# Optimization experiments

Measured on AMD Instinct MI355X. Metric: run time of the kernel, lower is better.

Reference implementation:

```python
import jax, jax.numpy as jnp
import numpy as np

EPS = 1e-6
NUM_HEADS = 16

def _ln(x):
    m = jnp.mean(x, -1, keepdims=True)
    v = jnp.mean((x - m) ** 2, -1, keepdims=True)
    return (x - m) * jax.lax.rsqrt(v + EPS)

def _rms(x, w):
    return x * jax.lax.rsqrt(jnp.mean(x * x, -1, keepdims=True) + EPS) * w

def _to_mha(t):
    B, S, D = t.shape
    return t.reshape(B, S, NUM_HEADS, D // NUM_HEADS).transpose(0, 2, 1, 3)

def _rope(t, freqs):
    # t: [B,H,T,Hd], freqs: [T, Hd//2, 2] (cos, sin)
    B, H, T, Hd = t.shape
    tr = t.reshape(B, H, T, Hd // 2, 2)
    cos, sin = freqs[..., 0], freqs[..., 1]
    r = tr[..., 0] * cos - tr[..., 1] * sin
    i = tr[..., 0] * sin + tr[..., 1] * cos
    return jnp.stack([r, i], -1).reshape(B, H, T, Hd)

def _pre(h, qk_w, qn, kn, v_w, v_b):
    qk = h @ qk_w.T                      # [B,S,2D], no bias (c_qk bias=False)
    q, k = jnp.split(qk, 2, -1)
    q = _rms(_to_mha(q), qn)             # per-head RMSNorm
    k = _rms(_to_mha(k), kn)
    v = _to_mha(h @ v_w.T + v_b)
    return q, k, v

def _post(x, a, pw, pb, w1, b1, w3, b3, w2, b2):
    x = x + a @ pw.T + pb                # residual + c_proj
    h = _ln(x)
    m = (jax.nn.silu(h @ w1.T + b1) * (h @ w3.T + b3)) @ w2.T + b2  # SwiGLU
    return x + m

def _forward(x, c, freqs, px_qk_w, px_qn, px_kn, px_v_w, px_v_b,
             pc_qk_w, pc_qn, pc_kn, pc_v_w, pc_v_b,
             p1_proj_w, p1_proj_b, p1_w1, p1_b1, p1_w3, p1_b3, p1_w2, p1_b2,
             p2_proj_w, p2_proj_b, p2_w1, p2_b1, p2_w3, p2_b3, p2_w2, p2_b2):
    x_ln, c_ln = _ln(x), _ln(c)
    qc, kc, vc = _pre(c_ln, pc_qk_w, pc_qn, pc_kn, pc_v_w, pc_v_b)
    qx, kx, vx = _pre(x_ln, px_qk_w, px_qn, px_kn, px_v_w, px_v_b)
    q = jnp.concatenate([qc, qx], 2)     # [B,H,T,Hd], T = S+L
    k = jnp.concatenate([kc, kx], 2)
    v = jnp.concatenate([vc, vx], 2)
    q = _rope(q, freqs)
    k = _rope(k, freqs)
    Hd = q.shape[-1]
    scores = jnp.einsum('bhqd,bhkd->bhqk', q, k) / jnp.sqrt(jnp.float32(Hd))
    T = scores.shape[-1]
    causal = jnp.tril(jnp.ones((T, T), bool))
    scores = jnp.where(causal, scores, jnp.finfo(scores.dtype).min)
    p = jax.nn.softmax(scores, -1)
    y = jnp.einsum('bhqk,bhkd->bhqd', p, v)
    B, D = x.shape[0], x.shape[-1]
    y = y.transpose(0, 2, 1, 3).reshape(B, -1, D)  # [B,T,D]
    S = c.shape[1]
    y_c, y_x = y[:, :S], y[:, S:]
    x_out = _post(x, y_x, p1_proj_w, p1_proj_b, p1_w1, p1_b1, p1_w3, p1_b3, p1_w2, p1_b2)
    c_out = _post(c, y_c, p2_proj_w, p2_proj_b, p2_w1, p2_b1, p2_w3, p2_b3, p2_w2, p2_b2)
    return x_out, c_out

def setup_inputs() -> dict:
    B, L, S, D, H, FF = 1, 1536, 512, 1024, 16, 4096
    Hd, T = D // H, L + S
    key = jax.random.key(0)
    ks = iter(jax.random.split(key, 40))
    def rn(shape, s=0.02):
        return (jax.random.normal(next(ks), shape, jnp.float32) * s)
    pos = jnp.arange(T, dtype=jnp.float32)
    inv = 1.0 / (10000.0 ** (jnp.arange(0, Hd, 2, dtype=jnp.float32) / Hd))
    ang = pos[:, None] * inv[None, :]
    freqs = jnp.stack([jnp.cos(ang), jnp.sin(ang)], -1)  # [T, Hd//2, 2]
    inp = {
        'x': jax.random.normal(next(ks), (B, L, D), jnp.float32),
        'c': jax.random.normal(next(ks), (B, S, D), jnp.float32),
        'freqs': freqs,
        'px_qk_w': rn((2 * D, D)), 'px_qn': jnp.ones((Hd,)), 'px_kn': jnp.ones((Hd,)),
        'px_v_w': rn((D, D)), 'px_v_b': rn((D,)),
        'pc_qk_w': rn((2 * D, D)), 'pc_qn': jnp.ones((Hd,)), 'pc_kn': jnp.ones((Hd,)),
        'pc_v_w': rn((D, D)), 'pc_v_b': rn((D,)),
    }
    for pfx in ('p1', 'p2'):
        inp[pfx + '_proj_w'] = rn((D, D)); inp[pfx + '_proj_b'] = rn((D,))
        inp[pfx + '_w1'] = rn((FF, D)); inp[pfx + '_b1'] = rn((FF,))
        inp[pfx + '_w3'] = rn((FF, D)); inp[pfx + '_b3'] = rn((FF,))
        inp[pfx + '_w2'] = rn((D, FF)); inp[pfx + '_b2'] = rn((D,))
    return inp

def reference(x, c, freqs, px_qk_w, px_qn, px_kn, px_v_w, px_v_b,
              pc_qk_w, pc_qn, pc_kn, pc_v_w, pc_v_b,
              p1_proj_w, p1_proj_b, p1_w1, p1_b1, p1_w3, p1_b3, p1_w2, p1_b2,
              p2_proj_w, p2_proj_b, p2_w1, p2_b1, p2_w3, p2_b3, p2_w2, p2_b2):
    return _forward(x, c, freqs, px_qk_w, px_qn, px_kn, px_v_w, px_v_b,
                    pc_qk_w, pc_qn, pc_kn, pc_v_w, pc_v_b,
                    p1_proj_w, p1_proj_b, p1_w1, p1_b1, p1_w3, p1_b3, p1_w2, p1_b2,
                    p2_proj_w, p2_proj_b, p2_w1, p2_b1, p2_w3, p2_b3, p2_w2, p2_b2)
```

## Files before the change

### kernel.cpp

```cpp
#include <hip/hip_runtime.h>

typedef __attribute__((ext_vector_type(8))) short short8;
typedef __attribute__((ext_vector_type(4))) float floatx4;
typedef __attribute__((ext_vector_type(4))) unsigned short ushortx4;

__device__ __forceinline__ float bf2f(unsigned short u) {
  union { unsigned int i; float f; } v; v.i = ((unsigned int)u) << 16; return v.f;
}
__device__ __forceinline__ unsigned short f2bf(float f) {
  union { float f; unsigned int i; } v; v.f = f;
  unsigned int x = v.i + 0x7fffu + ((v.i >> 16) & 1u);
  return (unsigned short)(x >> 16);
}
__device__ __forceinline__ float loadE(const void* p, size_t i, int f) {
  return f ? ((const float*)p)[i] : bf2f(((const unsigned short*)p)[i]);
}
__device__ __forceinline__ uint4 packbf(float4 a, float4 b) {
  union { unsigned short u[8]; uint4 v; } p;
  p.u[0] = f2bf(a.x); p.u[1] = f2bf(a.y); p.u[2] = f2bf(a.z); p.u[3] = f2bf(a.w);
  p.u[4] = f2bf(b.x); p.u[5] = f2bf(b.y); p.u[6] = f2bf(b.z); p.u[7] = f2bf(b.w);
  return p.v;
}

__device__ __forceinline__ void gl16(const unsigned short* g, unsigned short* l) {
  __builtin_amdgcn_global_load_lds(
      (const __attribute__((address_space(1))) void*)g,
      (__attribute__((address_space(3))) void*)l, 16, 0, 0);
}

__global__ void detect_kernel(const unsigned int* __restrict__ probe, int* __restrict__ flag) {
  if (threadIdx.x == 0 && blockIdx.x == 0) *flag = (probe[0] == 0x3F800000u) ? 1 : 0;
}

struct CArgs {
  const void* in[12];
  unsigned short* out[12];
  unsigned int cum[12];
};
__global__ __launch_bounds__(256) void convw_kernel(CArgs a, const int* __restrict__ flagp) {
  const int flag = *flagp;
  int bc = blockIdx.x * 2048;
  int s = 0;
  while (bc >= (int)a.cum[s]) ++s;
  int base = s ? (int)a.cum[s - 1] : 0;
  size_t e0 = ((size_t)(bc - base) + threadIdx.x) * 8;
  if (flag) {
    const float* in = (const float*)a.in[s];
    unsigned short* out = a.out[s];
    float4 v0[8], v1[8];
    #pragma unroll
    for (int k = 0; k < 8; ++k) {
      size_t e = e0 + (size_t)k * 2048;
      v0[k] = *(const float4*)(in + e);
      v1[k] = *(const float4*)(in + e + 4);
    }
    #pragma unroll
    for (int k = 0; k < 8; ++k)
      *(uint4*)(out + e0 + (size_t)k * 2048) = packbf(v0[k], v1[k]);
  } else {
    const unsigned short* in = (const unsigned short*)a.in[s];
    unsigned short* out = a.out[s];
    #pragma unroll
    for (int k = 0; k < 8; ++k) {
      size_t e = e0 + (size_t)k * 2048;
      *(uint4*)(out + e) = *(const uint4*)(in + e);
    }
  }
}

__global__ __launch_bounds__(256) void zero_kernel(void* __restrict__ out, int out_elems,
                                                   const int* __restrict__ flagp) {
  int limit = (*flagp) ? (out_elems >> 2) : (out_elems >> 3);
  int i = blockIdx.x * 256 + threadIdx.x;
  if (i < limit) ((uint4*)out)[i] = make_uint4(0, 0, 0, 0);
}

__global__ __launch_bounds__(256) void reduce_kernel(const float* __restrict__ part,
                                                     const unsigned short* __restrict__ mid,
                                                     const void* __restrict__ b1,
                                                     const void* __restrict__ b2,
                                                     float* __restrict__ out,
                                                     const int* __restrict__ flagp) {
  if (!*flagp) return;
  const size_t TD = 2097152, LD = (size_t)1536 * 1024, SD = (size_t)512 * 1024;
  size_t i = ((size_t)blockIdx.x * 256 + threadIdx.x) * 4;
  if (i >= TD) return;
  float4 v  = *(const float4*)(part + i);
  float4 v1 = *(const float4*)(part + TD + i);
  float4 v2 = *(const float4*)(part + 2 * TD + i);
  float4 v3 = *(const float4*)(part + 3 * TD + i);
  v.x += v1.x + v2.x + v3.x;
  v.y += v1.y + v2.y + v3.y;
  v.z += v1.z + v2.z + v3.z;
  v.w += v1.w + v2.w + v3.w;
  int col = (int)(i & 1023);
  const float* bias = (const float*)((i < LD) ? b1 : b2);
  size_t ri = (i < LD) ? (SD + i) : (i - LD);
  v.x += bias[col + 0] + bf2f(mid[ri + 0]);
  v.y += bias[col + 1] + bf2f(mid[ri + 1]);
  v.z += bias[col + 2] + bf2f(mid[ri + 2]);
  v.w += bias[col + 3] + bf2f(mid[ri + 3]);
  *(float4*)(out + i) = v;
}

__global__ __launch_bounds__(256) void reduce_mid_kernel(const float* __restrict__ part,
                                                         const void* __restrict__ cres,
                                                         const void* __restrict__ xres,
                                                         const float* __restrict__ b_c,
                                                         const float* __restrict__ b_x,
                                                         unsigned short* __restrict__ mid,
                                                         const int* __restrict__ flagp) {
  if (!*flagp) return;
  const size_t TD = 2097152;
  size_t i = ((size_t)blockIdx.x * 256 + threadIdx.x) * 4;
  if (i >= TD) return;
  float4 v  = *(const float4*)(part + i);
  float4 v1 = *(const float4*)(part + TD + i);
  float4 v2 = *(const float4*)(part + 2 * TD + i);
  float4 v3 = *(const float4*)(part + 3 * TD + i);
  v.x += v1.x + v2.x + v3.x;
  v.y += v1.y + v2.y + v3.y;
  v.z += v1.z + v2.z + v3.z;
  v.w += v1.w + v2.w + v3.w;
  int row = (int)(i >> 10), col = (int)(i & 1023);
  const float* bias = (row < 512) ? b_c : b_x;
  const float* res = (row < 512)
      ? (const float*)cres + ((size_t)row << 10) + col
      : (const float*)xres + ((size_t)(row - 512) << 10) + col;
  float4 rv = *(const float4*)res;
  float4 bv = *(const float4*)(bias + col);
  ushortx4 o;
  o[0] = f2bf(v.x + bv.x + rv.x);
  o[1] = f2bf(v.y + bv.y + rv.y);
  o[2] = f2bf(v.z + bv.z + rv.z);
  o[3] = f2bf(v.w + bv.w + rv.w);
  *(ushortx4*)(mid + i) = o;
}

__global__ __launch_bounds__(256) void ln_ext_kernel(const void* __restrict__ cin,
                                                     const void* __restrict__ xin,
                                                     unsigned short* __restrict__ out,
                                                     const int* __restrict__ flagp) {
  const int D = 1024, S = 512;
  const int flag = *flagp;
  int row = blockIdx.x;
  const void* src = (row < S) ? cin : xin;
  size_t rb = (size_t)(row < S ? row : row - S) * D;
  int base = threadIdx.x * 4;
  float x0 = loadE(src, rb + base + 0, flag);
  float x1 = loadE(src, rb + base + 1, flag);
  float x2 = loadE(src, rb + base + 2, flag);
  float x3 = loadE(src, rb + base + 3, flag);
  float s1 = x0 + x1 + x2 + x3;
  float s2 = x0 * x0 + x1 * x1 + x2 * x2 + x3 * x3;
  for (int off = 32; off; off >>= 1) {
    s1 += __shfl_down(s1, off, 64);
    s2 += __shfl_down(s2, off, 64);
  }
  __shared__ float red[8];
  int wid = threadIdx.x >> 6;
  if ((threadIdx.x & 63) == 0) { red[wid] = s1; red[4 + wid] = s2; }
  __syncthreads();
  s1 = red[0] + red[1] + red[2] + red[3];
  s2 = red[4] + red[5] + red[6] + red[7];
  float mean = s1 * (1.0f / D);
  float var = s2 * (1.0f / D) - mean * mean;
  float inv = rsqrtf(var + 1e-6f);
  unsigned short* dst = out + (size_t)row * D + base;
  dst[0] = f2bf((x0 - mean) * inv);
  dst[1] = f2bf((x1 - mean) * inv);
  dst[2] = f2bf((x2 - mean) * inv);
  dst[3] = f2bf((x3 - mean) * inv);
}

__global__ __launch_bounds__(256) void ln_mid_kernel(const unsigned short* __restrict__ in,
                                                     unsigned short* __restrict__ outc,
                                                     unsigned short* __restrict__ outx) {
  const int D = 1024, S = 512;
  int row = blockIdx.x;
  const unsigned short* src = in + (size_t)row * D;
  int base = threadIdx.x * 4;
  float x0 = bf2f(src[base + 0]);
  float x1 = bf2f(src[base + 1]);
  float x2 = bf2f(src[base + 2]);
  float x3 = bf2f(src[base + 3]);
  float s1 = x0 + x1 + x2 + x3;
  float s2 = x0 * x0 + x1 * x1 + x2 * x2 + x3 * x3;
  for (int off = 32; off; off >>= 1) {
    s1 += __shfl_down(s1, off, 64);
    s2 += __shfl_down(s2, off, 64);
  }
  __shared__ float red[8];
  int wid = threadIdx.x >> 6;
  if ((threadIdx.x & 63) == 0) { red[wid] = s1; red[4 + wid] = s2; }
  __syncthreads();
  s1 = red[0] + red[1] + red[2] + red[3];
  s2 = red[4] + red[5] + red[6] + red[7];
  float mean = s1 * (1.0f / D);
  float var = s2 * (1.0f / D) - mean * mean;
  float inv = rsqrtf(var + 1e-6f);
  unsigned short* dst = (row < S ? outc + (size_t)row * D : outx + (size_t)(row - S) * D) + base;
  dst[0] = f2bf((x0 - mean) * inv);
  dst[1] = f2bf((x1 - mean) * inv);
  dst[2] = f2bf((x2 - mean) * inv);
  dst[3] = f2bf((x3 - mean) * inv);
}

struct GArgs {
  const unsigned short* A[4];
  const void* B[4];
  const void* bias[4];
  const void* res[4];
  void* C[4];
  unsigned long long oo[4];
  int mcum[4];
  int N[4];
  int K;
  int nd;
  int tmask;
  float* part;
};

#define BAR() asm volatile("s_waitcnt lgkmcnt(0)\n\ts_barrier" ::: "memory")
#define FBAR() asm volatile("s_waitcnt vmcnt(0) lgkmcnt(0)\n\ts_barrier" ::: "memory")
#define CBAR4() asm volatile("s_waitcnt vmcnt(4) lgkmcnt(0)\n\ts_barrier" ::: "memory")

template <int RES_MODE, int OUT_MODE, int SPLITK, int BBF16>
__global__ __launch_bounds__(256) void gemm_kernel(GArgs g, const int* __restrict__ flagp) {
  const int flag = *flagp;
  int by = blockIdx.y;
  int d = 0;
  while (d < g.nd - 1 && by >= g.mcum[d]) ++d;
  int mbase = (d == 0) ? 0 : g.mcum[d - 1];
  const int m0 = (by - mbase) * 128;
  const int N = g.N[d];
  const int n0 = blockIdx.x * 128;
  if (n0 >= N) return;
  const int K = g.K;
  int kbeg = 0, kend = K;
  if (SPLITK > 1) {
    if (!flag) {
      if (blockIdx.z != 0) return;
    } else {
      int kl = K / SPLITK;
      kbeg = blockIdx.z * kl;
      kend = kbeg + kl;
    }
  }
  const int nt = (kend - kbeg) >> 5;

  constexpr int NBUF = BBF16 ? 3 : 2;
  constexpr int BSTRIDE = BBF16 ? 4096 : 5120;
  __shared__ __align__(16) unsigned short sA[NBUF * BSTRIDE];
  __shared__ __align__(16) unsigned short sB[NBUF * BSTRIDE];

  const int tid = threadIdx.x;
  const int lane = tid & 63;
  const int wave = tid >> 6;
  const int wm = (wave >> 1) * 64, wn = (wave & 1) * 64;
  const int srow = tid >> 2;
  const int scol = BBF16 ? ((((tid & 3) ^ ((tid >> 3) & 3))) * 8) : ((tid & 3) * 8);
  const unsigned short* Ag0 = g.A[d] + (size_t)(m0 + srow) * K + kbeg + scol;
  const unsigned short* Ag1 = Ag0 + (size_t)64 * K;
  const unsigned short* Bh0 = (const unsigned short*)g.B[d] + (size_t)(n0 + srow) * K + kbeg + scol;
  const unsigned short* Bh1 = Bh0 + (size_t)64 * K;

  const int fr = lane & 15;
  const int rdo = BBF16 ? ((((lane >> 4) ^ ((fr >> 1) & 3))) * 8) : ((lane >> 4) * 8);
  constexpr int PITCH = BBF16 ? 32 : 40;
  floatx4 acc[4][4] = {};
  auto compute = [&](const unsigned short* as, const unsigned short* bs) {
    short8 af[4], bfr[4];
    #pragma unroll
    for (int i = 0; i < 4; ++i) {
      af[i]  = *(const short8*)(as + (wm + i * 16 + fr) * PITCH + rdo);
      bfr[i] = *(const short8*)(bs + (wn + i * 16 + fr) * PITCH + rdo);
    }
    #pragma unroll
    for (int mi = 0; mi < 4; ++mi)
      #pragma unroll
      for (int ni = 0; ni < 4; ++ni)
        acc[mi][ni] = __builtin_amdgcn_mfma_f32_16x16x32_bf16(af[mi], bfr[ni], acc[mi][ni], 0, 0, 0);
  };

  if (BBF16) {
    unsigned short* lA0 = sA + wave * 512;
    unsigned short* lA1 = lA0 + 2048;
    unsigned short* lB0 = sB + wave * 512;
    unsigned short* lB1 = lB0 + 2048;
    auto stage = [&](int buf, int kk) {
      int bo = buf * 4096;
      gl16(Ag0 + kk, lA0 + bo);
      gl16(Ag1 + kk, lA1 + bo);
      gl16(Bh0 + kk, lB0 + bo);
      gl16(Bh1 + kk, lB1 + bo);
    };
    stage(0, 0);
    if (nt > 1) stage(1, 32);
    int b = 0;
    for (int t = 0; t < nt; ++t) {
      if (t + 1 < nt) CBAR4();
      else            FBAR();
      int b2 = (b >= 1) ? b - 1 : 2;
      if (t + 2 < nt) stage(b2, (t + 2) * 32);
      compute(sA + b * 4096, sB + b * 4096);
      b = (b == 2) ? 0 : b + 1;
    }
  } else {
    const float* Bf0 = (const float*)g.B[d] + (size_t)(n0 + srow) * K + kbeg + scol;
    const float* Bf1 = Bf0 + (size_t)64 * K;
    const int wo0 = srow * 40 + scol;
    const int wo1 = wo0 + 64 * 40;
    uint4 ra0, ra1, rb0, rb1;
    auto load_tile = [&](int kk) {
      ra0 = *(const uint4*)(Ag0 + kk);
      ra1 = *(const uint4*)(Ag1 + kk);
      if (!flag) {
        rb0 = *(const uint4*)(Bh0 + kk);
        rb1 = *(const uint4*)(Bh1 + kk);
      } else {
        float4 x0 = *(const float4*)(Bf0 + kk), x1 = *(const float4*)(Bf0 + kk + 4);
        float4 y0 = *(const float4*)(Bf1 + kk), y1 = *(const float4*)(Bf1 + kk + 4);
        rb0 = packbf(x0, x1);
        rb1 = packbf(y0, y1);
      }
    };
    auto store_tile = [&](int buf) {
      unsigned short* sa = sA + buf * 5120;
      unsigned short* sb = sB + buf * 5120;
      *(uint4*)(sa + wo0) = ra0;
      *(uint4*)(sa + wo1) = ra1;
      *(uint4*)(sb + wo0) = rb0;
      *(uint4*)(sb + wo1) = rb1;
    };
    load_tile(0);
    store_tile(0);
    if (nt > 1) load_tile(32);
    BAR();
    for (int t = 0; t < nt; ++t) {
      if (t + 1 < nt) {
        store_tile((t + 1) & 1);
        if (t + 2 < nt) load_tile((t + 2) * 32);
      }
      compute(sA + (t & 1) * 5120, sB + (t & 1) * 5120);
      if (t + 1 < nt) BAR();
    }
  }

  const void* bias = g.bias[d];
  const void* res = g.res[d];
  void* C = g.C[d];
  const size_t oo = g.oo[d];
  const bool first = (SPLITK <= 1) || (blockIdx.z == 0) || !flag;
  const bool rawpart = (OUT_MODE == 3) && (flag != 0);
  const bool trans = (OUT_MODE == 0) && (((g.tmask) >> d) & 1);
  #pragma unroll
  for (int mi = 0; mi < 4; ++mi)
    #pragma unroll
    for (int ni = 0; ni < 4; ++ni) {
      int colb = n0 + wn + ni * 16 + (lane & 15);
      int rowb = m0 + wm + mi * 16 + (lane >> 4) * 4;
      if (trans) {
        ushortx4 o4;
        #pragma unroll
        for (int r = 0; r < 4; ++r) {
          float val = acc[mi][ni][r];
          if (bias) val += loadE(bias, (size_t)colb, flag);
          o4[r] = f2bf(val);
        }
        *(ushortx4*)((unsigned short*)C + (size_t)colb * 2048 + oo + rowb) = o4;
      } else {
        #pragma unroll
        for (int r = 0; r < 4; ++r) {
          int row = rowb + r;
          int col = colb;
          float val = acc[mi][ni][r];
          size_t off = (size_t)row * N + col;
          if (first && !rawpart) {
            if (bias) val += loadE(bias, (size_t)col, flag);
            if (RES_MODE == 1) val += loadE(res, off, flag);
            if (RES_MODE == 3) {
              float h1v = bf2f(((const unsigned short*)res)[off]);
              val = (h1v / (1.0f + __expf(-h1v))) * val;
            }
            if (RES_MODE == 4) val += bf2f(((const unsigned short*)res)[off]);
          }
          if (OUT_MODE == 0) {
            ((unsigned short*)C)[off] = f2bf(val);
          } else if (OUT_MODE == 3) {
            if (flag) g.part[(size_t)blockIdx.z * 2097152 + oo + off] = val;
            else      ((unsigned short*)C)[oo + off] = f2bf(val);
          } else {
            if (flag) {
              if (SPLITK > 1) atomicAdd((float*)C + oo + off, val);
              else            ((float*)C)[oo + off] = val;
            } else {
              ((unsigned short*)C)[oo + off] = f2bf(val);
            }
          }
        }
      }
    }
}

__global__ __launch_bounds__(256) void rmsrope_kernel(
    unsigned short* __restrict__ qk,
    const void* __restrict__ qn_c, const void* __restrict__ kn_c,
    const void* __restrict__ qn_x, const void* __restrict__ kn_x,
    const void* __restrict__ freqs, const int* __restrict__ flagp) {
  const int flag = *flagp;
  int t = blockIdx.x;
  int h = blockIdx.y * 4 + (threadIdx.x >> 6);
  int d = threadIdx.x & 63;
  unsigned short* qrow = qk + (size_t)t * 2048 + h * 64;
  unsigned short* krow = qrow + 1024;
  float q = bf2f(qrow[d]), k = bf2f(krow[d]);
  float qs = q * q, ks = k * k;
  for (int off = 32; off; off >>= 1) {
    qs += __shfl_xor(qs, off, 64);
    ks += __shfl_xor(ks, off, 64);
  }
  const void* qn = (t < 512) ? qn_c : qn_x;
  const void* kn = (t < 512) ? kn_c : kn_x;
  q = q * rsqrtf(qs * (1.0f / 64.0f) + 1e-6f) * loadE(qn, d, flag);
  k = k * rsqrtf(ks * (1.0f / 64.0f) + 1e-6f) * loadE(kn, d, flag);
  int j = d >> 1;
  float cv = loadE(freqs, (size_t)(t * 32 + j) * 2 + 0, flag);
  float sv = loadE(freqs, (size_t)(t * 32 + j) * 2 + 1, flag);
  float qo = __shfl_xor(q, 1, 64);
  float ko = __shfl_xor(k, 1, 64);
  float qn2, kn2;
  if ((d & 1) == 0) { qn2 = q * cv - qo * sv; kn2 = k * cv - ko * sv; }
  else              { qn2 = qo * sv + q * cv; kn2 = ko * sv + k * cv; }
  qrow[d] = f2bf(qn2);
  krow[d] = f2bf(kn2);
}

__global__ __launch_bounds__(256) void attn_kernel(const unsigned short* __restrict__ qk,
                                                   const unsigned short* __restrict__ vT,
                                                   unsigned short* __restrict__ y) {
  int id = blockIdx.x;
  int blk = (id & 256) ? (31 - (id & 31)) : (id & 31);
  int h = (id >> 5) & 15;
  int wv = threadIdx.x >> 6;
  int lane = threadIdx.x & 63;
  int qbase = blk * 64 + wv * 16;

  __shared__ __align__(16) unsigned short Ks[2 * 4096];
  __shared__ __align__(16) unsigned short Vs[2 * 4096];
  __shared__ __align__(16) unsigned short ps[4][16 * 72];

  const int c0 = wv * 64 + lane;
  const int r0 = c0 >> 3,         k0 = (c0 & 7) ^ (r0 & 7);
  const int r1 = (c0 + 256) >> 3, k1 = (c0 & 7) ^ (r1 & 7);
  unsigned short* kd0 = Ks + wv * 512;
  unsigned short* kd1 = Ks + 2048 + wv * 512;
  unsigned short* vd0 = Vs + wv * 512;
  unsigned short* vd1 = Vs + 2048 + wv * 512;
  const unsigned short* kgp0 = qk + 1024 + h * 64 + k0 * 8 + (size_t)r0 * 2048;
  const unsigned short* kgp1 = qk + 1024 + h * 64 + k1 * 8 + (size_t)r1 * 2048;
  const unsigned short* vgp0 = vT + (size_t)(h * 64 + r0) * 2048 + k0 * 8;
  const unsigned short* vgp1 = vT + (size_t)(h * 64 + r1) * 2048 + k1 * 8;
  auto stage = [&](int buf, int j0) {
    int bo = buf * 4096;
    gl16(kgp0 + (size_t)j0 * 2048, kd0 + bo);
    gl16(kgp1 + (size_t)j0 * 2048, kd1 + bo);
    gl16(vgp0 + j0, vd0 + bo);
    gl16(vgp1 + j0, vd1 + bo);
  };

  short8 qa[2];
  {
    int m = lane & 15, dj = (lane >> 4) * 8;
    const unsigned short* qp = qk + (size_t)(qbase + m) * 2048 + h * 64 + dj;
    qa[0] = *(const short8*)(qp);
    qa[1] = *(const short8*)(qp + 32);
  }
  floatx4 o[4] = {};
  float mrow[4] = {-1e30f, -1e30f, -1e30f, -1e30f};
  float lrow[4] = {0.f, 0.f, 0.f, 0.f};
  int ntiles = blk + 1;

  stage(0, 0);
  FBAR();
  for (int tile = 0; tile < ntiles; ++tile) {
    int j0 = tile * 64;
    if (tile + 1 < ntiles) stage((tile + 1) & 1, j0 + 64);
    const unsigned short* Kb = Ks + (tile & 1) * 4096;
    const unsigned short* Vb = Vs + (tile & 1) * 4096;
    floatx4 sacc[4];
    #pragma unroll
    for (int kg = 0; kg < 4; ++kg) {
      floatx4 z = {0.f, 0.f, 0.f, 0.f};
      #pragma unroll
      for (int kc = 0; kc < 2; ++kc) {
        int kr = kg * 16 + (lane & 15);
        int p = (kc * 4 + (lane >> 4)) ^ (kr & 7);
        short8 kb = *(const short8*)(Kb + kr * 64 + p * 8);
        z = __builtin_amdgcn_mfma_f32_16x16x32_bf16(qa[kc], kb, z, 0, 0, 0);
      }
      sacc[kg] = z;
    }
    if (tile == blk) {
      #pragma unroll
      for (int kg = 0; kg < 4; ++kg)
        #pragma unroll
        for (int r = 0; r < 4; ++r) {
          int key_g = j0 + kg * 16 + (lane & 15);
          int q_g = qbase + (lane >> 4) * 4 + r;
          float s = sacc[kg][r] * 0.125f;
          sacc[kg][r] = (key_g <= q_g) ? s : -1e30f;
        }
    } else {
      #pragma unroll
      for (int kg = 0; kg < 4; ++kg)
        #pragma unroll
        for (int r = 0; r < 4; ++r) sacc[kg][r] *= 0.125f;
    }
    #pragma unroll
    for (int r = 0; r < 4; ++r) {
      float mx = fmaxf(fmaxf(sacc[0][r], sacc[1][r]), fmaxf(sacc[2][r], sacc[3][r]));
      mx = fmaxf(mx, __shfl_xor(mx, 1, 64));
      mx = fmaxf(mx, __shfl_xor(mx, 2, 64));
      mx = fmaxf(mx, __shfl_xor(mx, 4, 64));
      mx = fmaxf(mx, __shfl_xor(mx, 8, 64));
      float mnew = fmaxf(mrow[r], mx);
      float al = __expf(mrow[r] - mnew);
      mrow[r] = mnew;
      float sum = 0.f;
      #pragma unroll
      for (int kg = 0; kg < 4; ++kg) {
        float p = __expf(sacc[kg][r] - mnew);
        sacc[kg][r] = p;
        sum += p;
      }
      sum += __shfl_xor(sum, 1, 64);
      sum += __shfl_xor(sum, 2, 64);
      sum += __shfl_xor(sum, 4, 64);
      sum += __shfl_xor(sum, 8, 64);
      lrow[r] = lrow[r] * al + sum;
      #pragma unroll
      for (int ni = 0; ni < 4; ++ni) o[ni][r] *= al;
    }
    unsigned short* pw = ps[wv];
    #pragma unroll
    for (int kg = 0; kg < 4; ++kg)
      #pragma unroll
      for (int r = 0; r < 4; ++r)
        pw[((lane >> 4) * 4 + r) * 72 + kg * 16 + (lane & 15)] = f2bf(sacc[kg][r]);
    asm volatile("s_waitcnt lgkmcnt(0)" ::: "memory");
    short8 pa[2];
    pa[0] = *(const short8*)(pw + (lane & 15) * 72 + (lane >> 4) * 8);
    pa[1] = *(const short8*)(pw + (lane & 15) * 72 + 32 + (lane >> 4) * 8);
    #pragma unroll
    for (int ni = 0; ni < 4; ++ni) {
      floatx4 z = o[ni];
      int dd = ni * 16 + (lane & 15);
      #pragma unroll
      for (int kc = 0; kc < 2; ++kc) {
        int p = (kc * 4 + (lane >> 4)) ^ (dd & 7);
        short8 vb = *(const short8*)(Vb + dd * 64 + p * 8);
        z = __builtin_amdgcn_mfma_f32_16x16x32_bf16(pa[kc], vb, z, 0, 0, 0);
      }
      o[ni] = z;
    }
    if (tile + 1 < ntiles) FBAR();
  }
  #pragma unroll
  for (int ni = 0; ni < 4; ++ni)
    #pragma unroll
    for (int r = 0; r < 4; ++r) {
      int q = qbase + (lane >> 4) * 4 + r;
      int dd = ni * 16 + (lane & 15);
      y[(size_t)q * 1024 + h * 64 + dd] = f2bf(o[ni][r] / lrow[r]);
    }
}

extern "C" void kernel_launch(void* const* d_in, const int* in_sizes, int n_in,
                              void* d_out, int out_size, void* d_ws, size_t ws_size,
                              hipStream_t stream) {
  const int L = 1536, S = 512, D = 1024, T = 2048, FF = 4096;
  const void* x        = d_in[0];
  const void* c        = d_in[1];
  const void* freqs    = d_in[2];
  const void* px_qk_w  = d_in[3];
  const void* px_qn    = d_in[4];
  const void* px_kn    = d_in[5];
  const void* px_v_w   = d_in[6];
  const void* px_v_b   = d_in[7];
  const void* pc_qk_w  = d_in[8];
  const void* pc_qn    = d_in[9];
  const void* pc_kn    = d_in[10];
  const void* pc_v_w   = d_in[11];
  const void* pc_v_b   = d_in[12];
  const void* p1_proj_w = d_in[13];
  const void* p1_proj_b = d_in[14];
  const void* p1_w1 = d_in[15];
  const void* p1_b1 = d_in[16];
  const void* p1_w3 = d_in[17];
  const void* p1_b3 = d_in[18];
  const void* p1_w2 = d_in[19];
  const void* p1_b2 = d_in[20];
  const void* p2_proj_w = d_in[21];
  const void* p2_proj_b = d_in[22];
  const void* p2_w1 = d_in[23];
  const void* p2_b1 = d_in[24];
  const void* p2_w3 = d_in[25];
  const void* p2_b3 = d_in[26];
  const void* p2_w2 = d_in[27];
  const void* p2_b2 = d_in[28];

  char* ws = (char*)d_ws;
  unsigned short* hln     = (unsigned short*)(ws);
  unsigned short* ybuf    = (unsigned short*)(ws);
  unsigned short* h1c     = (unsigned short*)(ws);
  unsigned short* qkbuf   = (unsigned short*)(ws + ((size_t)4  << 20));
  unsigned short* h1x     = (unsigned short*)(ws + ((size_t)4  << 20));
  unsigned short* vbufT   = (unsigned short*)(ws + ((size_t)12 << 20));
  unsigned short* mid     = (unsigned short*)(ws + ((size_t)16 << 20));
  unsigned short* midln_c = (unsigned short*)(ws + ((size_t)20 << 20));
  int*            flag    = (int*)(ws + ((size_t)21 << 20));
  unsigned short* midln_x = (unsigned short*)d_out;
  unsigned short* hlnx    = hln + (size_t)S * D;

  const bool conv = ws_size >= ((size_t)90 << 20);
  unsigned short* wbf = (unsigned short*)(ws + ((size_t)24 << 20));
  unsigned short* b_qk_c = wbf + 0;
  unsigned short* b_qk_x = wbf + 2097152;
  unsigned short* b_v_c  = wbf + 4194304;
  unsigned short* b_v_x  = wbf + 5242880;
  unsigned short* b_pj1  = wbf + 6291456;
  unsigned short* b_pj2  = wbf + 7340032;
  unsigned short* b_w1p1 = wbf + 8388608;
  unsigned short* b_w1p2 = wbf + 12582912;
  unsigned short* b_w3p1 = wbf + 16777216;
  unsigned short* b_w3p2 = wbf + 20971520;
  unsigned short* b_w2p1 = wbf + 25165824;
  unsigned short* b_w2p2 = wbf + 29360128;
  float* part = (float*)(ws + ((size_t)40 << 20));

  detect_kernel<<<1, 64, 0, stream>>>((const unsigned int*)px_qn, flag);

  if (conv) {
    CArgs ca = {};
    const void* insA[8]    = {pc_qk_w, px_qk_w, pc_v_w, px_v_w, p1_proj_w, p2_proj_w,
                              p1_w2, p2_w2};
    unsigned short* osA[8] = {b_qk_c, b_qk_x, b_v_c, b_v_x, b_pj1, b_pj2,
                              b_w2p1, b_w2p2};
    unsigned int cntA[8]   = {262144, 262144, 131072, 131072, 131072, 131072,
                              524288, 524288};
    unsigned int cum = 0;
    for (int i = 0; i < 8; ++i) { ca.in[i] = insA[i]; ca.out[i] = osA[i]; cum += cntA[i]; ca.cum[i] = cum; }
    for (int i = 8; i < 12; ++i) ca.cum[i] = 0x7FFFFFFFu;
    convw_kernel<<<1024, 256, 0, stream>>>(ca, flag);
  }

  ln_ext_kernel<<<T, 256, 0, stream>>>(c, x, hln, flag);

  {
    GArgs g = {};
    g.A[0] = hln;  g.bias[0] = nullptr; g.C[0] = qkbuf;                    g.mcum[0] = 4;  g.N[0] = 2048;
    g.A[1] = hlnx; g.bias[1] = nullptr; g.C[1] = qkbuf + (size_t)S * 2048; g.mcum[1] = 16; g.N[1] = 2048;
    g.A[2] = hln;  g.bias[2] = pc_v_b;  g.C[2] = vbufT; g.oo[2] = 0;       g.mcum[2] = 20; g.N[2] = 1024;
    g.A[3] = hlnx; g.bias[3] = px_v_b;  g.C[3] = vbufT; g.oo[3] = S;       g.mcum[3] = 32; g.N[3] = 1024;
    g.K = 1024; g.nd = 4; g.tmask = 0b1100;
    if (conv) {
      g.B[0] = b_qk_c; g.B[1] = b_qk_x; g.B[2] = b_v_c; g.B[3] = b_v_x;
      gemm_kernel<0, 0, 1, 1><<<dim3(16, 32), 256, 0, stream>>>(g, flag);
    } else {
      g.B[0] = pc_qk_w; g.B[1] = px_qk_w; g.B[2] = pc_v_w; g.B[3] = px_v_w;
      gemm_kernel<0, 0, 1, 0><<<dim3(16, 32), 256, 0, stream>>>(g, flag);
    }
  }
  rmsrope_kernel<<<dim3(T, 4), 256, 0, stream>>>(qkbuf, pc_qn, pc_kn, px_qn, px_kn, freqs, flag);
  attn_kernel<<<512, 256, 0, stream>>>(qkbuf, vbufT, ybuf);

  if (conv) {
    GArgs g = {};
    g.A[0] = ybuf;                  g.C[0] = mid; g.oo[0] = 0;             g.bias[0] = p2_proj_b; g.res[0] = c; g.mcum[0] = 4;  g.N[0] = 1024;
    g.A[1] = ybuf + (size_t)S * D;  g.C[1] = mid; g.oo[1] = (size_t)S * D; g.bias[1] = p1_proj_b; g.res[1] = x; g.mcum[1] = 16; g.N[1] = 1024;
    g.K = 1024; g.nd = 2;
    g.part = part;
    g.B[0] = b_pj2; g.B[1] = b_pj1;
    gemm_kernel<1, 3, 4, 1><<<dim3(8, 16, 4), 256, 0, stream>>>(g, flag);
    reduce_mid_kernel<<<2048, 256, 0, stream>>>(part, c, x, (const float*)p2_proj_b,
                                                (const float*)p1_proj_b, mid, flag);
    CArgs cb = {};
    const void* insB[4]    = {p1_w1, p2_w1, p1_w3, p2_w3};
    unsigned short* osB[4] = {b_w1p1, b_w1p2, b_w3p1, b_w3p2};
    unsigned int cum = 0;
    for (int i = 0; i < 4; ++i) { cb.in[i] = insB[i]; cb.out[i] = osB[i]; cum += 524288u; cb.cum[i] = cum; }
    for (int i = 4; i < 12; ++i) cb.cum[i] = 0x7FFFFFFFu;
    convw_kernel<<<1024, 256, 0, stream>>>(cb, flag);
  } else {
    GArgs g = {};
    g.A[0] = ybuf;                  g.bias[0] = p2_proj_b; g.res[0] = c; g.C[0] = mid;                  g.mcum[0] = 4;  g.N[0] = 1024;
    g.A[1] = ybuf + (size_t)S * D;  g.bias[1] = p1_proj_b; g.res[1] = x; g.C[1] = mid + (size_t)S * D;  g.mcum[1] = 16; g.N[1] = 1024;
    g.K = 1024; g.nd = 2;
    g.B[0] = p2_proj_w; g.B[1] = p1_proj_w;
    gemm_kernel<1, 0, 1, 0><<<dim3(8, 16), 256, 0, stream>>>(g, flag);
  }
  ln_mid_kernel<<<T, 256, 0, stream>>>(mid, midln_c, midln_x);

  {
    GArgs g = {};
    g.A[0] = midln_x; g.bias[0] = p1_b1; g.C[0] = h1x; g.mcum[0] = 12; g.N[0] = 4096;
    g.A[1] = midln_c; g.bias[1] = p2_b1; g.C[1] = h1c; g.mcum[1] = 16; g.N[1] = 4096;
    g.K = 1024; g.nd = 2;
    if (conv) {
      g.B[0] = b_w1p1; g.B[1] = b_w1p2;
      gemm_kernel<0, 0, 1, 1><<<dim3(32, 16), 256, 0, stream>>>(g, flag);
    } else {
      g.B[0] = p1_w1; g.B[1] = p2_w1;
      gemm_kernel<0, 0, 1, 0><<<dim3(32, 16), 256, 0, stream>>>(g, flag);
    }
  }
  {
    GArgs g = {};
    g.A[0] = midln_x; g.bias[0] = p1_b3; g.res[0] = h1x; g.C[0] = h1x; g.mcum[0] = 12; g.N[0] = 4096;
    g.A[1] = midln_c; g.bias[1] = p2_b3; g.res[1] = h1c; g.C[1] = h1c; g.mcum[1] = 16; g.N[1] = 4096;
    g.K = 1024; g.nd = 2;
    if (conv) {
      g.B[0] = b_w3p1; g.B[1] = b_w3p2;
      gemm_kernel<3, 0, 1, 1><<<dim3(32, 16), 256, 0, stream>>>(g, flag);
    } else {
      g.B[0] = p1_w3; g.B[1] = p2_w3;
      gemm_kernel<3, 0, 1, 0><<<dim3(32, 16), 256, 0, stream>>>(g, flag);
    }
  }
  if (conv) {
    GArgs g = {};
    g.A[0] = h1x; g.bias[0] = p1_b2; g.res[0] = mid + (size_t)S * D; g.C[0] = d_out; g.oo[0] = 0;             g.mcum[0] = 12; g.N[0] = 1024;
    g.A[1] = h1c; g.bias[1] = p2_b2; g.res[1] = mid;                 g.C[1] = d_out; g.oo[1] = (size_t)L * D; g.mcum[1] = 16; g.N[1] = 1024;
    g.K = 4096; g.nd = 2;
    g.part = part;
    g.B[0] = b_w2p1; g.B[1] = b_w2p2;
    gemm_kernel<4, 3, 4, 1><<<dim3(8, 16, 4), 256, 0, stream>>>(g, flag);
    reduce_kernel<<<2048, 256, 0, stream>>>(part, mid, p1_b2, p2_b2, (float*)d_out, flag);
  } else {
    zero_kernel<<<2048, 256, 0, stream>>>(d_out, out_size, flag);
    GArgs g = {};
    g.A[0] = h1x; g.bias[0] = p1_b2; g.res[0] = mid + (size_t)S * D; g.C[0] = d_out; g.oo[0] = 0;             g.mcum[0] = 12; g.N[0] = 1024;
    g.A[1] = h1c; g.bias[1] = p2_b2; g.res[1] = mid;                 g.C[1] = d_out; g.oo[1] = (size_t)L * D; g.mcum[1] = 16; g.N[1] = 1024;
    g.K = 4096; g.nd = 2;
    g.B[0] = p1_w2; g.B[1] = p2_w2;
    gemm_kernel<4, 2, 4, 0><<<dim3(8, 16, 4), 256, 0, stream>>>(g, flag);
  }
}
```

Baseline: 485.6 us.

## Split causal attention across KV chunks with a separate combine kernel

Attention is split along the key dimension into chunks of up to 8 tiles per query block, launched as a 3D grid with up to 4 splits. Each split writes its unnormalized output and running max/sum to workspace, and a new combine kernel merges them with a log-sum-exp rescale. The aim is to even out the causal imbalance and raise the block count so the GPU stays occupied. In exchange it adds fp32 partial traffic, an extra launch, and drops the old pairing of long and short query blocks.

```diff
diff --git a/kernel.cpp b/kernel.cpp
--- a/kernel.cpp
+++ b/kernel.cpp
@@ -436,15 +436,23 @@
   krow[d] = f2bf(kn2);
 }
 
+template <int SPLIT>
 __global__ __launch_bounds__(256) void attn_kernel(const unsigned short* __restrict__ qk,
                                                    const unsigned short* __restrict__ vT,
-                                                   unsigned short* __restrict__ y) {
-  int id = blockIdx.x;
-  int blk = (id & 256) ? (31 - (id & 31)) : (id & 31);
-  int h = (id >> 5) & 15;
+                                                   unsigned short* __restrict__ y,
+                                                   float* __restrict__ opart,
+                                                   float* __restrict__ mlpart) {
+  int qblk = blockIdx.x;
+  int h = blockIdx.y;
+  int z = SPLIT ? blockIdx.z : 0;
+  int ntiles = qblk + 1;
+  int t0 = z * 8;
+  if (SPLIT && t0 >= ntiles) return;
+  int t1 = SPLIT ? (t0 + 8 < ntiles ? t0 + 8 : ntiles) : ntiles;
+  int ns = SPLIT ? ((qblk + 8) >> 3) : 1;
   int wv = threadIdx.x >> 6;
   int lane = threadIdx.x & 63;
-  int qbase = blk * 64 + wv * 16;
+  int qbase = qblk * 64 + wv * 16;
 
   __shared__ __align__(16) unsigned short Ks[2 * 4096];
   __shared__ __align__(16) unsigned short Vs[2 * 4096];
@@ -479,29 +487,29 @@
   floatx4 o[4] = {};
   float mrow[4] = {-1e30f, -1e30f, -1e30f, -1e30f};
   float lrow[4] = {0.f, 0.f, 0.f, 0.f};
-  int ntiles = blk + 1;
-
-  stage(0, 0);
+
+  stage(0, t0 * 64);
   FBAR();
-  for (int tile = 0; tile < ntiles; ++tile) {
+  for (int tile = t0; tile < t1; ++tile) {
     int j0 = tile * 64;
-    if (tile + 1 < ntiles) stage((tile + 1) & 1, j0 + 64);
-    const unsigned short* Kb = Ks + (tile & 1) * 4096;
-    const unsigned short* Vb = Vs + (tile & 1) * 4096;
+    int ti = tile - t0;
+    if (tile + 1 < t1) stage((ti + 1) & 1, j0 + 64);
+    const unsigned short* Kb = Ks + (ti & 1) * 4096;
+    const unsigned short* Vb = Vs + (ti & 1) * 4096;
     floatx4 sacc[4];
     #pragma unroll
     for (int kg = 0; kg < 4; ++kg) {
-      floatx4 z = {0.f, 0.f, 0.f, 0.f};
+      floatx4 zz = {0.f, 0.f, 0.f, 0.f};
       #pragma unroll
       for (int kc = 0; kc < 2; ++kc) {
         int kr = kg * 16 + (lane & 15);
         int p = (kc * 4 + (lane >> 4)) ^ (kr & 7);
         short8 kb = *(const short8*)(Kb + kr * 64 + p * 8);
-        z = __builtin_amdgcn_mfma_f32_16x16x32_bf16(qa[kc], kb, z, 0, 0, 0);
+        zz = __builtin_amdgcn_mfma_f32_16x16x32_bf16(qa[kc], kb, zz, 0, 0, 0);
       }
-      sacc[kg] = z;
-    }
-    if (tile == blk) {
+      sacc[kg] = zz;
+    }
+    if (tile == qblk) {
       #pragma unroll
       for (int kg = 0; kg < 4; ++kg)
         #pragma unroll
@@ -554,26 +562,94 @@
     pa[1] = *(const short8*)(pw + (lane & 15) * 72 + 32 + (lane >> 4) * 8);
     #pragma unroll
     for (int ni = 0; ni < 4; ++ni) {
-      floatx4 z = o[ni];
+      floatx4 zz = o[ni];
       int dd = ni * 16 + (lane & 15);
       #pragma unroll
       for (int kc = 0; kc < 2; ++kc) {
         int p = (kc * 4 + (lane >> 4)) ^ (dd & 7);
         short8 vb = *(const short8*)(Vb + dd * 64 + p * 8);
-        z = __builtin_amdgcn_mfma_f32_16x16x32_bf16(pa[kc], vb, z, 0, 0, 0);
+        zz = __builtin_amdgcn_mfma_f32_16x16x32_bf16(pa[kc], vb, zz, 0, 0, 0);
       }
-      o[ni] = z;
-    }
-    if (tile + 1 < ntiles) FBAR();
-  }
+      o[ni] = zz;
+    }
+    if (tile + 1 < t1) FBAR();
+  }
+
+  if (ns == 1) {
+    #pragma unroll
+    for (int ni = 0; ni < 4; ++ni)
+      #pragma unroll
+      for (int r = 0; r < 4; ++r) {
+        int q = qbase + (lane >> 4) * 4 + r;
+        int dd = ni * 16 + (lane & 15);
+        y[(size_t)q * 1024 + h * 64 + dd] = f2bf(o[ni][r] / lrow[r]);
+      }
+  } else {
+    float* op = opart + ((size_t)((qblk << 4) + h) * 4 + z) * 4096;
+    #pragma unroll
+    for (int ni = 0; ni < 4; ++ni)
+      #pragma unroll
+      for (int r = 0; r < 4; ++r) {
+        int row = wv * 16 + (lane >> 4) * 4 + r;
+        int col = ni * 16 + (lane & 15);
+        op[row * 64 + col] = o[ni][r];
+      }
+    float* mlp = mlpart + ((size_t)((qblk << 4) + h) * 4 + z) * 128;
+    if ((lane & 15) == 0) {
+      #pragma unroll
+      for (int r = 0; r < 4; ++r) {
+        int row = wv * 16 + (lane >> 4) * 4 + r;
+        mlp[row] = mrow[r];
+        mlp[64 + row] = lrow[r];
+      }
+    }
+  }
+}
+
+__global__ __launch_bounds__(256) void attn_combine_kernel(const float* __restrict__ opart,
+                                                           const float* __restrict__ mlpart,
+                                                           unsigned short* __restrict__ y) {
+  int g = blockIdx.x;
+  int qblk = g >> 4, h = g & 15;
+  int ns = (qblk + 8) >> 3;
+  if (ns < 2) return;
+  int row = threadIdx.x >> 2;
+  int col0 = (threadIdx.x & 3) << 4;
+  const float* mlg = mlpart + (size_t)g * 512;
+  float m0v = mlg[row],       l0v = mlg[64 + row];
+  float m1v = mlg[128 + row], l1v = mlg[192 + row];
+  float m2v = (ns > 2) ? mlg[256 + row] : -1e30f;
+  float l2v = (ns > 2) ? mlg[320 + row] : 0.f;
+  float m3v = (ns > 3) ? mlg[384 + row] : -1e30f;
+  float l3v = (ns > 3) ? mlg[448 + row] : 0.f;
+  float M = fmaxf(fmaxf(m0v, m1v), fmaxf(m2v, m3v));
+  float w0 = __expf(m0v - M), w1 = __expf(m1v - M);
+  float w2 = (ns > 2) ? __expf(m2v - M) : 0.f;
+  float w3 = (ns > 3) ? __expf(m3v - M) : 0.f;
+  float inv = 1.0f / (w0 * l0v + w1 * l1v + w2 * l2v + w3 * l3v);
+  const float* og = opart + (size_t)g * 16384 + row * 64 + col0;
+  unsigned short* yp = y + (size_t)(qblk * 64 + row) * 1024 + h * 64 + col0;
   #pragma unroll
-  for (int ni = 0; ni < 4; ++ni)
-    #pragma unroll
-    for (int r = 0; r < 4; ++r) {
-      int q = qbase + (lane >> 4) * 4 + r;
-      int dd = ni * 16 + (lane & 15);
-      y[(size_t)q * 1024 + h * 64 + dd] = f2bf(o[ni][r] / lrow[r]);
-    }
+  for (int j = 0; j < 16; j += 4) {
+    float4 v0 = *(const float4*)(og + j);
+    float4 v1 = *(const float4*)(og + 4096 + j);
+    float ax = w0 * v0.x + w1 * v1.x;
+    float ay = w0 * v0.y + w1 * v1.y;
+    float az = w0 * v0.z + w1 * v1.z;
+    float aw = w0 * v0.w + w1 * v1.w;
+    if (ns > 2) {
+      float4 v2 = *(const float4*)(og + 8192 + j);
+      ax += w2 * v2.x; ay += w2 * v2.y; az += w2 * v2.z; aw += w2 * v2.w;
+    }
+    if (ns > 3) {
+      float4 v3 = *(const float4*)(og + 12288 + j);
+      ax += w3 * v3.x; ay += w3 * v3.y; az += w3 * v3.z; aw += w3 * v3.w;
+    }
+    ushortx4 o4;
+    o4[0] = f2bf(ax * inv); o4[1] = f2bf(ay * inv);
+    o4[2] = f2bf(az * inv); o4[3] = f2bf(aw * inv);
+    *(ushortx4*)(yp + j) = o4;
+  }
 }
 
 extern "C" void kernel_launch(void* const* d_in, const int* in_sizes, int n_in,
@@ -620,6 +696,7 @@
   unsigned short* mid     = (unsigned short*)(ws + ((size_t)16 << 20));
   unsigned short* midln_c = (unsigned short*)(ws + ((size_t)20 << 20));
   int*            flag    = (int*)(ws + ((size_t)21 << 20));
+  float*          mlpart  = (float*)(ws + ((size_t)22 << 20));
   unsigned short* midln_x = (unsigned short*)d_out;
   unsigned short* hlnx    = hln + (size_t)S * D;
 
@@ -637,7 +714,8 @@
   unsigned short* b_w3p2 = wbf + 20971520;
   unsigned short* b_w2p1 = wbf + 25165824;
   unsigned short* b_w2p2 = wbf + 29360128;
-  float* part = (float*)(ws + ((size_t)40 << 20));
+  float* part  = (float*)(ws + ((size_t)40 << 20));
+  float* opart = (float*)(ws + ((size_t)40 << 20));
 
   detect_kernel<<<1, 64, 0, stream>>>((const unsigned int*)px_qn, flag);
 
@@ -673,7 +751,12 @@
     }
   }
   rmsrope_kernel<<<dim3(T, 4), 256, 0, stream>>>(qkbuf, pc_qn, pc_kn, px_qn, px_kn, freqs, flag);
-  attn_kernel<<<512, 256, 0, stream>>>(qkbuf, vbufT, ybuf);
+  if (conv) {
+    attn_kernel<1><<<dim3(32, 16, 4), 256, 0, stream>>>(qkbuf, vbufT, ybuf, opart, mlpart);
+    attn_combine_kernel<<<512, 256, 0, stream>>>(opart, mlpart, ybuf);
+  } else {
+    attn_kernel<0><<<dim3(32, 16, 1), 256, 0, stream>>>(qkbuf, vbufT, ybuf, opart, mlpart);
+  }
 
   if (conv) {
     GArgs g = {};
```

New measurement: 494.8 us. No clear change (+1.9%).
